# Optimization experiments

Hardware: AMD Instinct MI355X
Metric: run time of the kernel (lower is better)

Reference implementation:

```python
import jax, jax.numpy as jnp
import numpy as np

B, S, D = 64, 512, 768
NEG = -1e30


def setup_inputs() -> dict:
    key = jax.random.key(0)
    ks = jax.random.split(key, 20)
    def rn(k, shape, scale=0.02):
        return jax.random.normal(k, shape, dtype=jnp.float32) * scale
    ep = jax.random.randint(ks[1], (B, 3, 2), 0, S, dtype=jnp.int32)
    return {
        "encoding": jax.random.normal(ks[0], (B, S, D), dtype=jnp.float32),
        "ent_pos": jnp.sort(ep, axis=-1),
        "Ar_W": rn(ks[2], (5, D)), "Ar_b": rn(ks[3], (D,)),
        "Vr_W1": rn(ks[4], (2 * D, 512)), "Vr_b1": rn(ks[5], (512,)),
        "Vr_W2": rn(ks[6], (512, 5)), "Vr_b2": rn(ks[7], (5,)),
        "gate_W": rn(ks[8], (2 * D, D)), "gate_b": rn(ks[9], (D,)),
        "pred_W1": rn(ks[10], (3 * D, 512)), "pred_b1": rn(ks[11], (512,)),
        "pred_W2": rn(ks[12], (512, 5)), "pred_b2": rn(ks[13], (5,)),
        "proj_W": rn(ks[14], (D, 1)), "proj_b": rn(ks[15], (1,)),
    }


def reference(encoding, ent_pos, Ar_W, Ar_b, Vr_W1, Vr_b1, Vr_W2, Vr_b2,
              gate_W, gate_b, pred_W1, pred_b1, pred_W2, pred_b2, proj_W, proj_b):
    # --- entity span max-pooling (vectorized over batch & 3 entities) ---
    pos = jnp.arange(S)                                   # [S]
    start = ent_pos[..., 0:1]                             # [B,3,1]
    end = ent_pos[..., 1:2]                               # [B,3,1]
    mask = (pos >= start) & (pos <= end)                  # [B,3,S]
    ent = jnp.max(jnp.where(mask[..., None], encoding[:, None, :, :], NEG), axis=2)  # [B,3,D]
    # dropout layers are identity at inference

    def vr(a, b):  # V_r_layer: Linear(1536,512)+ReLU+Linear(512,5)+Sigmoid
        h = jax.nn.relu(jnp.concatenate([a, b], axis=-1) @ Vr_W1 + Vr_b1)
        return jax.nn.sigmoid(h @ Vr_W2 + Vr_b2)          # [B,5]

    def gate(u, e):  # gated residual update
        g = jax.nn.sigmoid(jnp.concatenate([u, e], axis=-1) @ gate_W + gate_b)
        return g * e + (1.0 - g) * u

    e1, e2, e3 = ent[:, 0], ent[:, 1], ent[:, 2]          # [B,D] each
    for _ in range(5):
        u1 = (vr(e2, e3) @ Ar_W + Ar_b) * e1
        u2 = (vr(e1, e3) @ Ar_W + Ar_b) * e2
        u3 = (vr(e1, e2) @ Ar_W + Ar_b) * e3
        e1, e2, e3 = gate(u1, e1), gate(u2, e2), gate(u3, e3)
    final_ent = jnp.stack([e1, e2, e3], axis=1)           # [B,3,D]

    # predict_layer on the ORIGINAL pooled entity embeddings (per source code)
    flat = ent.reshape(B, 3 * D)
    rel = jax.nn.relu(flat @ pred_W1 + pred_b1) @ pred_W2 + pred_b2  # [B,5]
    ent_score = jax.nn.sigmoid(ent @ proj_W + proj_b)[..., 0]       # [B,3]
    return rel, ent_score, final_ent
```

## Files before the change

kernel.cpp:

```cpp
#include <hip/hip_runtime.h>
#include <hip/hip_bf16.h>
#include <math.h>

#define NEGF (-1e30f)

#define P_OFF    0u
#define PP_OFF   0u
#define ENT_OFF  2359296u
#define EA_OFF   2506752u
#define EB_OFF   2654208u
#define SP_OFF   2801664u

__device__ __forceinline__ float sigmoidf_(float x){ return 1.0f/(1.0f+expf(-x)); }

__global__ __launch_bounds__(192) void k_span_partial(
    const float* __restrict__ enc, const int* __restrict__ ent_pos, float* __restrict__ ws)
{
    int c = blockIdx.x, bi = blockIdx.y, t = threadIdx.x;
    int b = bi/3;
    int st = ent_pos[bi*2+0], en = ent_pos[bi*2+1];
    int r0 = max(st, c*32), r1 = min(en, c*32+31);
    if (r0 > r1) return;
    float4 m = make_float4(NEGF,NEGF,NEGF,NEGF);
    const float4* e4 = (const float4*)enc + (size_t)b*512*192 + t;
    int r = r0;
    for (; r+3<=r1; r+=4){
        float4 v0 = e4[(size_t)(r  )*192];
        float4 v1 = e4[(size_t)(r+1)*192];
        float4 v2 = e4[(size_t)(r+2)*192];
        float4 v3 = e4[(size_t)(r+3)*192];
        m.x=fmaxf(m.x,fmaxf(fmaxf(v0.x,v1.x),fmaxf(v2.x,v3.x)));
        m.y=fmaxf(m.y,fmaxf(fmaxf(v0.y,v1.y),fmaxf(v2.y,v3.y)));
        m.z=fmaxf(m.z,fmaxf(fmaxf(v0.z,v1.z),fmaxf(v2.z,v3.z)));
        m.w=fmaxf(m.w,fmaxf(fmaxf(v0.w,v1.w),fmaxf(v2.w,v3.w)));
    }
    for (; r<=r1; ++r){
        float4 v = e4[(size_t)r*192];
        m.x=fmaxf(m.x,v.x); m.y=fmaxf(m.y,v.y); m.z=fmaxf(m.z,v.z); m.w=fmaxf(m.w,v.w);
    }
    ((float4*)(ws+P_OFF))[((size_t)bi*16 + c)*192 + t] = m;
}

__global__ __launch_bounds__(192) void k_span_reduce(
    const int* __restrict__ ent_pos,
    const float* __restrict__ projW, const float* __restrict__ projb,
    float* __restrict__ ws, float* __restrict__ out)
{
    __shared__ float red[4];
    int bi = blockIdx.x; int t = threadIdx.x;
    int st = ent_pos[bi*2+0], en = ent_pos[bi*2+1];
    float4 m = make_float4(NEGF,NEGF,NEGF,NEGF);
    const float4* p4 = (const float4*)(ws+P_OFF);
    for (int c=0;c<16;++c){
        if (c*32 <= en && c*32+31 >= st){
            float4 v = p4[((size_t)bi*16 + c)*192 + t];
            m.x=fmaxf(m.x,v.x); m.y=fmaxf(m.y,v.y); m.z=fmaxf(m.z,v.z); m.w=fmaxf(m.w,v.w);
        }
    }
    ((float4*)(ws+ENT_OFF))[bi*192+t] = m;
    ((float4*)(ws+EA_OFF))[bi*192+t] = m;
    float4 w = ((const float4*)projW)[t];
    float v = m.x*w.x + m.y*w.y + m.z*w.z + m.w*w.w;
    v += __shfl_down(v, 32);
    v += __shfl_down(v, 16);
    v += __shfl_down(v, 8);
    v += __shfl_down(v, 4);
    v += __shfl_down(v, 2);
    v += __shfl_down(v, 1);
    if ((t & 63) == 0) red[t>>6] = v;
    __syncthreads();
    if (t==0) out[320 + bi] = sigmoidf_(red[0]+red[1]+red[2] + projb[0]);
}

__global__ __launch_bounds__(256) void k_pred_part(
    const float* __restrict__ predW1, float* __restrict__ ws)
{
    int ct = blockIdx.x, rb = blockIdx.y, ks = blockIdx.z;
    int tx = threadIdx.x & 31, ty = threadIdx.x >> 5;
    int row = rb*8+ty, col = ct*32+tx;
    const float* A = ws + ENT_OFF + (size_t)row*2304 + ks*288;
    const float* W = predW1 + (size_t)(ks*288)*512 + col;
    float acc = 0.f;
    #pragma unroll 4
    for (int k=0;k<288;++k){ acc = fmaf(A[k], W[(size_t)k*512], acc); }
    ws[PP_OFF + ((size_t)(ks*64+row))*512 + col] = acc;
}

__global__ __launch_bounds__(256) void k_vr_fused(
    const float* __restrict__ W1, const float* __restrict__ b1,
    const float* __restrict__ W2, const float* __restrict__ eSrc,
    const float* __restrict__ pb1, const float* __restrict__ pW2,
    const float* __restrict__ pb2,
    float* __restrict__ ws, float* __restrict__ out)
{
    __shared__ float eL[4608];
    __shared__ float red[16*16*17];
    int g = blockIdx.x;
    int t = threadIdx.x;
    if (g >= 256){
        int bx = g - 256;
        int gid = t >> 5, l = t & 31;
        int b = bx*8 + gid;
        float acc0=0,acc1=0,acc2=0,acc3=0,acc4=0;
        for (int c = l; c < 512; c += 32){
            float h = 0.f;
            #pragma unroll
            for (int ks=0;ks<8;++ks) h += ws[PP_OFF + ((size_t)(ks*64+b))*512 + c];
            h = fmaxf(h + pb1[c], 0.f);
            acc0 = fmaf(h, pW2[c*5+0], acc0);
            acc1 = fmaf(h, pW2[c*5+1], acc1);
            acc2 = fmaf(h, pW2[c*5+2], acc2);
            acc3 = fmaf(h, pW2[c*5+3], acc3);
            acc4 = fmaf(h, pW2[c*5+4], acc4);
        }
        #pragma unroll
        for (int s=16; s>0; s>>=1){
            acc0 += __shfl_down(acc0, s, 32);
            acc1 += __shfl_down(acc1, s, 32);
            acc2 += __shfl_down(acc2, s, 32);
            acc3 += __shfl_down(acc3, s, 32);
            acc4 += __shfl_down(acc4, s, 32);
        }
        if (l == 0){
            out[b*5+0] = acc0 + pb2[0];
            out[b*5+1] = acc1 + pb2[1];
            out[b*5+2] = acc2 + pb2[2];
            out[b*5+3] = acc3 + pb2[3];
            out[b*5+4] = acc4 + pb2[4];
        }
        return;
    }
    int ct = g & 7, bg = g >> 3;
    int b0 = bg*2;
    const float* eBase = eSrc + (size_t)b0*2304;
    for (int idx=t; idx<4608; idx+=256) eL[idx] = eBase[idx];
    __syncthreads();

    int tp = t & 15;
    int kq = t >> 4;
    int c0 = ct*64;
    int col = c0 + 4*tp;
    const float* Wp = W1 + (size_t)(kq*96)*512 + col;
    int off1 = (kq<8) ? (768 + kq*96) : (1536 + (kq-8)*96);
    int off2 = (kq<8) ? (      kq*96) : (768  + (kq-8)*96);
    const float* pP0 = eL + off1;
    const float* pQ0 = eL + off2;
    const float* pP1 = eL + 2304 + off1;
    const float* pQ1 = eL + 2304 + off2;
    float aP0[4]={0,0,0,0}, aQ0[4]={0,0,0,0}, aP1[4]={0,0,0,0}, aQ1[4]={0,0,0,0};
    #pragma unroll 8
    for (int i=0;i<96;++i){
        float4 w = *(const float4*)(Wp + (size_t)i*512);
        float p0 = pP0[i], q0 = pQ0[i], p1 = pP1[i], q1 = pQ1[i];
        aP0[0]=fmaf(p0,w.x,aP0[0]); aP0[1]=fmaf(p0,w.y,aP0[1]); aP0[2]=fmaf(p0,w.z,aP0[2]); aP0[3]=fmaf(p0,w.w,aP0[3]);
        aQ0[0]=fmaf(q0,w.x,aQ0[0]); aQ0[1]=fmaf(q0,w.y,aQ0[1]); aQ0[2]=fmaf(q0,w.z,aQ0[2]); aQ0[3]=fmaf(q0,w.w,aQ0[3]);
        aP1[0]=fmaf(p1,w.x,aP1[0]); aP1[1]=fmaf(p1,w.y,aP1[1]); aP1[2]=fmaf(p1,w.z,aP1[2]); aP1[3]=fmaf(p1,w.w,aP1[3]);
        aQ1[0]=fmaf(q1,w.x,aQ1[0]); aQ1[1]=fmaf(q1,w.y,aQ1[1]); aQ1[2]=fmaf(q1,w.z,aQ1[2]); aQ1[3]=fmaf(q1,w.w,aQ1[3]);
    }
    float* rp = red + (kq*16 + tp)*17;
    #pragma unroll
    for (int c=0;c<4;++c){ rp[c]=aP0[c]; rp[4+c]=aQ0[c]; rp[8+c]=aP1[c]; rp[12+c]=aQ1[c]; }
    __syncthreads();

    if (t < 128){
        int bb = t >> 6;
        int tc = t & 63;
        int tp2 = tc >> 2, c = tc & 3;
        int base = bb*8;
        float SP1=0,SP2=0,SQ1=0,SQ2=0;
        #pragma unroll
        for (int k=0;k<8;++k){
            SP1 += red[(k*16+tp2)*17 + base + c];
            SQ1 += red[(k*16+tp2)*17 + base + 4 + c];
            SP2 += red[((k+8)*16+tp2)*17 + base + c];
            SQ2 += red[((k+8)*16+tp2)*17 + base + 4 + c];
        }
        int cc = c0 + tc;
        float bv = b1[cc];
        float h0 = fmaxf(SP1+SP2+bv, 0.f);
        float h1 = fmaxf(SQ1+SP2+bv, 0.f);
        float h2 = fmaxf(SQ1+SQ2+bv, 0.f);
        float w20 = W2[cc*5+0], w21 = W2[cc*5+1], w22 = W2[cc*5+2], w23 = W2[cc*5+3], w24 = W2[cc*5+4];
        float pr[15] = { h0*w20,h0*w21,h0*w22,h0*w23,h0*w24,
                         h1*w20,h1*w21,h1*w22,h1*w23,h1*w24,
                         h2*w20,h2*w21,h2*w22,h2*w23,h2*w24 };
        #pragma unroll
        for (int j=0;j<15;++j){
            float v = pr[j];
            v += __shfl_down(v, 32);
            v += __shfl_down(v, 16);
            v += __shfl_down(v, 8);
            v += __shfl_down(v, 4);
            v += __shfl_down(v, 2);
            v += __shfl_down(v, 1);
            pr[j] = v;
        }
        if (tc == 0){
            float* sp = ws + SP_OFF + ((size_t)ct*192 + (size_t)(b0+bb)*3)*5;
            #pragma unroll
            for (int j=0;j<15;++j) sp[j] = pr[j];
        }
    }
}

__global__ __launch_bounds__(384) void k_gate_fused(
    const float* __restrict__ gW, const float* __restrict__ gb,
    const float* __restrict__ ArW, const float* __restrict__ Arb,
    const float* __restrict__ Vb2,
    const float* __restrict__ eSrc, float* __restrict__ eDst,
    float* __restrict__ ws, float* __restrict__ finalOut)
{
    __shared__ float eL[4608];
    __shared__ float uL[4608];
    __shared__ float red[16*24*25];
    __shared__ float sL[32];
    int g = blockIdx.x;
    int t = threadIdx.x;
    int ct = g & 7, bg = g >> 3;
    int b0 = bg*2;
    const float* eBase = eSrc + (size_t)b0*2304;
    for (int idx=t; idx<4608; idx+=384) eL[idx] = eBase[idx];
    if (t < 30){
        int bb = t/15, pc = t%15, cc = pc%5;
        int row = (b0+bb)*3 + pc/5;
        float pre = Vb2[cc];
        #pragma unroll
        for (int q=0;q<8;++q) pre += ws[SP_OFF + ((size_t)q*192 + row)*5 + cc];
        sL[t] = sigmoidf_(pre);
    }
    __syncthreads();
    for (int idx=t; idx<4608; idx+=384){
        int r = idx / 768;
        int k = idx - r*768;
        int bb = r / 3;  int p = r - bb*3;
        const float* s = sL + bb*15 + p*5;
        float a = Arb[k] + s[0]*ArW[k] + s[1]*ArW[768+k] + s[2]*ArW[1536+k]
                         + s[3]*ArW[2304+k] + s[4]*ArW[3072+k];
        uL[idx] = a * eL[idx];
    }
    __syncthreads();

    int kq = t / 24, tp = t - kq*24;
    int c0 = ct*96;
    int col = c0 + 4*tp;
    const float* Wp = gW + (size_t)(kq*96)*768 + col;
    const float* A = (kq<8) ? uL : eL;
    int kb = (kq & 7)*96;
    float acc[6][4];
    #pragma unroll
    for (int r=0;r<6;++r){ acc[r][0]=0.f; acc[r][1]=0.f; acc[r][2]=0.f; acc[r][3]=0.f; }
    #pragma unroll 4
    for (int i=0;i<96;++i){
        float4 w = *(const float4*)(Wp + (size_t)i*768);
        #pragma unroll
        for (int r=0;r<6;++r){
            float a = A[r*768 + kb + i];
            acc[r][0] = fmaf(a, w.x, acc[r][0]);
            acc[r][1] = fmaf(a, w.y, acc[r][1]);
            acc[r][2] = fmaf(a, w.z, acc[r][2]);
            acc[r][3] = fmaf(a, w.w, acc[r][3]);
        }
    }
    float* rp = red + (kq*24+tp)*25;
    #pragma unroll
    for (int r=0;r<6;++r){
        rp[r*4+0]=acc[r][0]; rp[r*4+1]=acc[r][1]; rp[r*4+2]=acc[r][2]; rp[r*4+3]=acc[r][3];
    }
    __syncthreads();

    for (int o=t; o<576; o+=384){
        int rr = o / 96, tc = o - rr*96;
        int tp2 = tc >> 2, c = tc & 3;
        int bb = rr/3, p = rr - bb*3;
        float gp = 0.f;
        #pragma unroll
        for (int k=0;k<16;++k) gp += red[(k*24+tp2)*25 + rr*4 + c];
        int jc = c0 + tc;
        float gv = sigmoidf_(gp + gb[jc]);
        float e = eL[bb*2304 + p*768 + jc];
        float u = uL[bb*2304 + p*768 + jc];
        float val = gv*e + (1.f-gv)*u;
        size_t oi = ((size_t)(b0+bb)*3 + p)*768 + jc;
        eDst[oi] = val;
        if (finalOut) finalOut[oi] = val;
    }
}

extern "C" void kernel_launch(void* const* d_in, const int* in_sizes, int n_in,
                              void* d_out, int out_size, void* d_ws, size_t ws_size,
                              hipStream_t stream)
{
    const float* enc     = (const float*)d_in[0];
    const int*   ent_pos = (const int*)d_in[1];
    const float* ArW     = (const float*)d_in[2];
    const float* Arb     = (const float*)d_in[3];
    const float* VrW1    = (const float*)d_in[4];
    const float* Vrb1    = (const float*)d_in[5];
    const float* VrW2    = (const float*)d_in[6];
    const float* Vrb2    = (const float*)d_in[7];
    const float* gateW   = (const float*)d_in[8];
    const float* gateb   = (const float*)d_in[9];
    const float* predW1  = (const float*)d_in[10];
    const float* predb1  = (const float*)d_in[11];
    const float* predW2  = (const float*)d_in[12];
    const float* predb2  = (const float*)d_in[13];
    const float* projW   = (const float*)d_in[14];
    const float* projb   = (const float*)d_in[15];
    float* out = (float*)d_out;
    float* ws  = (float*)d_ws;

    hipLaunchKernelGGL(k_span_partial, dim3(16,192), dim3(192), 0, stream, enc, ent_pos, ws);
    hipLaunchKernelGGL(k_span_reduce, dim3(192), dim3(192), 0, stream, ent_pos, projW, projb, ws, out);
    hipLaunchKernelGGL(k_pred_part, dim3(16,8,8), dim3(256), 0, stream, predW1, ws);
    for (int it=0; it<5; ++it){
        float* eS = ws + ((it&1)==0 ? EA_OFF : EB_OFF);
        float* eD = ws + ((it&1)==0 ? EB_OFF : EA_OFF);
        hipLaunchKernelGGL(k_vr_fused, dim3(it==0 ? 264 : 256), dim3(256), 0, stream,
                           VrW1, Vrb1, VrW2, eS, predb1, predW2, predb2, ws, out);
        hipLaunchKernelGGL(k_gate_fused, dim3(256), dim3(384), 0, stream, gateW, gateb, ArW, Arb, Vrb2,
                           eS, eD, ws, (it==4) ? (out+512) : (float*)nullptr);
    }
}
```

Baseline: 160.2 us.

## Use one batch per block in vr/gate kernels and fold pred GEMM into first vr launch

The vr and gate kernels now give each block one batch row instead of two, which doubles the grid to 512 blocks and halves shared memory and register accumulators. This should improve occupancy and spread work over more CUs, at the cost of loading each weight tile twice as often. The separate predict-layer partial GEMM is folded into the first vr launch as extra blocks, and a small new kernel finishes the prediction head after it. The gate kernel gains an unused dead-code branch for blocks at index 512 and above, but it never runs because only 512 blocks are launched.

```diff
diff --git a/kernel.cpp b/kernel.cpp
--- a/kernel.cpp
+++ b/kernel.cpp
@@ -72,68 +72,32 @@
     if (t==0) out[320 + bi] = sigmoidf_(red[0]+red[1]+red[2] + projb[0]);
 }
 
-__global__ __launch_bounds__(256) void k_pred_part(
-    const float* __restrict__ predW1, float* __restrict__ ws)
-{
-    int ct = blockIdx.x, rb = blockIdx.y, ks = blockIdx.z;
-    int tx = threadIdx.x & 31, ty = threadIdx.x >> 5;
-    int row = rb*8+ty, col = ct*32+tx;
-    const float* A = ws + ENT_OFF + (size_t)row*2304 + ks*288;
-    const float* W = predW1 + (size_t)(ks*288)*512 + col;
-    float acc = 0.f;
-    #pragma unroll 4
-    for (int k=0;k<288;++k){ acc = fmaf(A[k], W[(size_t)k*512], acc); }
-    ws[PP_OFF + ((size_t)(ks*64+row))*512 + col] = acc;
-}
-
 __global__ __launch_bounds__(256) void k_vr_fused(
     const float* __restrict__ W1, const float* __restrict__ b1,
     const float* __restrict__ W2, const float* __restrict__ eSrc,
-    const float* __restrict__ pb1, const float* __restrict__ pW2,
-    const float* __restrict__ pb2,
-    float* __restrict__ ws, float* __restrict__ out)
-{
-    __shared__ float eL[4608];
-    __shared__ float red[16*16*17];
+    const float* __restrict__ pW1,
+    float* __restrict__ ws)
+{
+    __shared__ float eL[2304];
+    __shared__ float red[16*16*9];
     int g = blockIdx.x;
     int t = threadIdx.x;
-    if (g >= 256){
-        int bx = g - 256;
-        int gid = t >> 5, l = t & 31;
-        int b = bx*8 + gid;
-        float acc0=0,acc1=0,acc2=0,acc3=0,acc4=0;
-        for (int c = l; c < 512; c += 32){
-            float h = 0.f;
-            #pragma unroll
-            for (int ks=0;ks<8;++ks) h += ws[PP_OFF + ((size_t)(ks*64+b))*512 + c];
-            h = fmaxf(h + pb1[c], 0.f);
-            acc0 = fmaf(h, pW2[c*5+0], acc0);
-            acc1 = fmaf(h, pW2[c*5+1], acc1);
-            acc2 = fmaf(h, pW2[c*5+2], acc2);
-            acc3 = fmaf(h, pW2[c*5+3], acc3);
-            acc4 = fmaf(h, pW2[c*5+4], acc4);
-        }
-        #pragma unroll
-        for (int s=16; s>0; s>>=1){
-            acc0 += __shfl_down(acc0, s, 32);
-            acc1 += __shfl_down(acc1, s, 32);
-            acc2 += __shfl_down(acc2, s, 32);
-            acc3 += __shfl_down(acc3, s, 32);
-            acc4 += __shfl_down(acc4, s, 32);
-        }
-        if (l == 0){
-            out[b*5+0] = acc0 + pb2[0];
-            out[b*5+1] = acc1 + pb2[1];
-            out[b*5+2] = acc2 + pb2[2];
-            out[b*5+3] = acc3 + pb2[3];
-            out[b*5+4] = acc4 + pb2[4];
-        }
+    if (g >= 512){
+        int g2 = g - 512;
+        int ct2 = g2 & 15, rb = (g2 >> 4) & 7, ks = g2 >> 7;
+        int tx = t & 31, ty = t >> 5;
+        int row = rb*8+ty, col = ct2*32+tx;
+        const float* A = ws + ENT_OFF + (size_t)row*2304 + ks*288;
+        const float* W = pW1 + (size_t)(ks*288)*512 + col;
+        float acc = 0.f;
+        #pragma unroll 4
+        for (int k=0;k<288;++k){ acc = fmaf(A[k], W[(size_t)k*512], acc); }
+        ws[PP_OFF + ((size_t)(ks*64+row))*512 + col] = acc;
         return;
     }
-    int ct = g & 7, bg = g >> 3;
-    int b0 = bg*2;
-    const float* eBase = eSrc + (size_t)b0*2304;
-    for (int idx=t; idx<4608; idx+=256) eL[idx] = eBase[idx];
+    int ct = g & 7, b = g >> 3;
+    const float* eBase = eSrc + (size_t)b*2304;
+    for (int idx=t; idx<2304; idx+=256) eL[idx] = eBase[idx];
     __syncthreads();
 
     int tp = t & 15;
@@ -143,37 +107,31 @@
     const float* Wp = W1 + (size_t)(kq*96)*512 + col;
     int off1 = (kq<8) ? (768 + kq*96) : (1536 + (kq-8)*96);
     int off2 = (kq<8) ? (      kq*96) : (768  + (kq-8)*96);
-    const float* pP0 = eL + off1;
-    const float* pQ0 = eL + off2;
-    const float* pP1 = eL + 2304 + off1;
-    const float* pQ1 = eL + 2304 + off2;
-    float aP0[4]={0,0,0,0}, aQ0[4]={0,0,0,0}, aP1[4]={0,0,0,0}, aQ1[4]={0,0,0,0};
+    const float* pP = eL + off1;
+    const float* pQ = eL + off2;
+    float aP[4]={0,0,0,0}, aQ[4]={0,0,0,0};
     #pragma unroll 8
     for (int i=0;i<96;++i){
         float4 w = *(const float4*)(Wp + (size_t)i*512);
-        float p0 = pP0[i], q0 = pQ0[i], p1 = pP1[i], q1 = pQ1[i];
-        aP0[0]=fmaf(p0,w.x,aP0[0]); aP0[1]=fmaf(p0,w.y,aP0[1]); aP0[2]=fmaf(p0,w.z,aP0[2]); aP0[3]=fmaf(p0,w.w,aP0[3]);
-        aQ0[0]=fmaf(q0,w.x,aQ0[0]); aQ0[1]=fmaf(q0,w.y,aQ0[1]); aQ0[2]=fmaf(q0,w.z,aQ0[2]); aQ0[3]=fmaf(q0,w.w,aQ0[3]);
-        aP1[0]=fmaf(p1,w.x,aP1[0]); aP1[1]=fmaf(p1,w.y,aP1[1]); aP1[2]=fmaf(p1,w.z,aP1[2]); aP1[3]=fmaf(p1,w.w,aP1[3]);
-        aQ1[0]=fmaf(q1,w.x,aQ1[0]); aQ1[1]=fmaf(q1,w.y,aQ1[1]); aQ1[2]=fmaf(q1,w.z,aQ1[2]); aQ1[3]=fmaf(q1,w.w,aQ1[3]);
-    }
-    float* rp = red + (kq*16 + tp)*17;
+        float p = pP[i], q = pQ[i];
+        aP[0]=fmaf(p,w.x,aP[0]); aP[1]=fmaf(p,w.y,aP[1]); aP[2]=fmaf(p,w.z,aP[2]); aP[3]=fmaf(p,w.w,aP[3]);
+        aQ[0]=fmaf(q,w.x,aQ[0]); aQ[1]=fmaf(q,w.y,aQ[1]); aQ[2]=fmaf(q,w.z,aQ[2]); aQ[3]=fmaf(q,w.w,aQ[3]);
+    }
+    float* rp = red + (kq*16 + tp)*9;
     #pragma unroll
-    for (int c=0;c<4;++c){ rp[c]=aP0[c]; rp[4+c]=aQ0[c]; rp[8+c]=aP1[c]; rp[12+c]=aQ1[c]; }
-    __syncthreads();
-
-    if (t < 128){
-        int bb = t >> 6;
-        int tc = t & 63;
+    for (int c=0;c<4;++c){ rp[c]=aP[c]; rp[4+c]=aQ[c]; }
+    __syncthreads();
+
+    if (t < 64){
+        int tc = t;
         int tp2 = tc >> 2, c = tc & 3;
-        int base = bb*8;
         float SP1=0,SP2=0,SQ1=0,SQ2=0;
         #pragma unroll
         for (int k=0;k<8;++k){
-            SP1 += red[(k*16+tp2)*17 + base + c];
-            SQ1 += red[(k*16+tp2)*17 + base + 4 + c];
-            SP2 += red[((k+8)*16+tp2)*17 + base + c];
-            SQ2 += red[((k+8)*16+tp2)*17 + base + 4 + c];
+            SP1 += red[(k*16+tp2)*9 + c];
+            SQ1 += red[(k*16+tp2)*9 + 4 + c];
+            SP2 += red[((k+8)*16+tp2)*9 + c];
+            SQ2 += red[((k+8)*16+tp2)*9 + 4 + c];
         }
         int cc = c0 + tc;
         float bv = b1[cc];
@@ -196,7 +154,7 @@
             pr[j] = v;
         }
         if (tc == 0){
-            float* sp = ws + SP_OFF + ((size_t)ct*192 + (size_t)(b0+bb)*3)*5;
+            float* sp = ws + SP_OFF + ((size_t)ct*192 + (size_t)b*3)*5;
             #pragma unroll
             for (int j=0;j<15;++j) sp[j] = pr[j];
         }
@@ -207,33 +165,67 @@
     const float* __restrict__ gW, const float* __restrict__ gb,
     const float* __restrict__ ArW, const float* __restrict__ Arb,
     const float* __restrict__ Vb2,
+    const float* __restrict__ pb1, const float* __restrict__ pW2,
+    const float* __restrict__ pb2,
     const float* __restrict__ eSrc, float* __restrict__ eDst,
     float* __restrict__ ws, float* __restrict__ finalOut)
 {
-    __shared__ float eL[4608];
-    __shared__ float uL[4608];
-    __shared__ float red[16*24*25];
-    __shared__ float sL[32];
+    __shared__ float eL[2304];
+    __shared__ float uL[2304];
+    __shared__ float red[16*24*13];
+    __shared__ float sL[16];
     int g = blockIdx.x;
     int t = threadIdx.x;
-    int ct = g & 7, bg = g >> 3;
-    int b0 = bg*2;
-    const float* eBase = eSrc + (size_t)b0*2304;
-    for (int idx=t; idx<4608; idx+=384) eL[idx] = eBase[idx];
-    if (t < 30){
-        int bb = t/15, pc = t%15, cc = pc%5;
-        int row = (b0+bb)*3 + pc/5;
+    if (g >= 512){
+        int bx = g - 512;
+        int gid = t >> 5, l = t & 31;
+        if (gid < 8){
+            int b = bx*8 + gid;
+            float acc0=0,acc1=0,acc2=0,acc3=0,acc4=0;
+            for (int c = l; c < 512; c += 32){
+                float h = 0.f;
+                #pragma unroll
+                for (int ks=0;ks<8;++ks) h += ws[PP_OFF + ((size_t)(ks*64+b))*512 + c];
+                h = fmaxf(h + pb1[c], 0.f);
+                acc0 = fmaf(h, pW2[c*5+0], acc0);
+                acc1 = fmaf(h, pW2[c*5+1], acc1);
+                acc2 = fmaf(h, pW2[c*5+2], acc2);
+                acc3 = fmaf(h, pW2[c*5+3], acc3);
+                acc4 = fmaf(h, pW2[c*5+4], acc4);
+            }
+            #pragma unroll
+            for (int s=16; s>0; s>>=1){
+                acc0 += __shfl_down(acc0, s, 32);
+                acc1 += __shfl_down(acc1, s, 32);
+                acc2 += __shfl_down(acc2, s, 32);
+                acc3 += __shfl_down(acc3, s, 32);
+                acc4 += __shfl_down(acc4, s, 32);
+            }
+            if (l == 0){
+                float* o = finalOut ? finalOut : finalOut;
+                (void)o;
+            }
+            if (l == 0){
+            }
+        }
+        return;
+    }
+    int ct = g & 7, b = g >> 3;
+    const float* eBase = eSrc + (size_t)b*2304;
+    for (int idx=t; idx<2304; idx+=384) eL[idx] = eBase[idx];
+    if (t < 15){
+        int cc = t%5, p = t/5;
+        int row = b*3 + p;
         float pre = Vb2[cc];
         #pragma unroll
         for (int q=0;q<8;++q) pre += ws[SP_OFF + ((size_t)q*192 + row)*5 + cc];
         sL[t] = sigmoidf_(pre);
     }
     __syncthreads();
-    for (int idx=t; idx<4608; idx+=384){
+    for (int idx=t; idx<2304; idx+=384){
         int r = idx / 768;
         int k = idx - r*768;
-        int bb = r / 3;  int p = r - bb*3;
-        const float* s = sL + bb*15 + p*5;
+        const float* s = sL + r*5;
         float a = Arb[k] + s[0]*ArW[k] + s[1]*ArW[768+k] + s[2]*ArW[1536+k]
                          + s[3]*ArW[2304+k] + s[4]*ArW[3072+k];
         uL[idx] = a * eL[idx];
@@ -246,14 +238,14 @@
     const float* Wp = gW + (size_t)(kq*96)*768 + col;
     const float* A = (kq<8) ? uL : eL;
     int kb = (kq & 7)*96;
-    float acc[6][4];
+    float acc[3][4];
     #pragma unroll
-    for (int r=0;r<6;++r){ acc[r][0]=0.f; acc[r][1]=0.f; acc[r][2]=0.f; acc[r][3]=0.f; }
+    for (int r=0;r<3;++r){ acc[r][0]=0.f; acc[r][1]=0.f; acc[r][2]=0.f; acc[r][3]=0.f; }
     #pragma unroll 4
     for (int i=0;i<96;++i){
         float4 w = *(const float4*)(Wp + (size_t)i*768);
         #pragma unroll
-        for (int r=0;r<6;++r){
+        for (int r=0;r<3;++r){
             float a = A[r*768 + kb + i];
             acc[r][0] = fmaf(a, w.x, acc[r][0]);
             acc[r][1] = fmaf(a, w.y, acc[r][1]);
@@ -261,28 +253,63 @@
             acc[r][3] = fmaf(a, w.w, acc[r][3]);
         }
     }
-    float* rp = red + (kq*24+tp)*25;
+    float* rp = red + (kq*24+tp)*13;
     #pragma unroll
-    for (int r=0;r<6;++r){
+    for (int r=0;r<3;++r){
         rp[r*4+0]=acc[r][0]; rp[r*4+1]=acc[r][1]; rp[r*4+2]=acc[r][2]; rp[r*4+3]=acc[r][3];
     }
     __syncthreads();
 
-    for (int o=t; o<576; o+=384){
-        int rr = o / 96, tc = o - rr*96;
+    if (t < 288){
+        int rr = t / 96, tc = t - rr*96;
         int tp2 = tc >> 2, c = tc & 3;
-        int bb = rr/3, p = rr - bb*3;
         float gp = 0.f;
         #pragma unroll
-        for (int k=0;k<16;++k) gp += red[(k*24+tp2)*25 + rr*4 + c];
+        for (int k=0;k<16;++k) gp += red[(k*24+tp2)*13 + rr*4 + c];
         int jc = c0 + tc;
         float gv = sigmoidf_(gp + gb[jc]);
-        float e = eL[bb*2304 + p*768 + jc];
-        float u = uL[bb*2304 + p*768 + jc];
+        float e = eL[rr*768 + jc];
+        float u = uL[rr*768 + jc];
         float val = gv*e + (1.f-gv)*u;
-        size_t oi = ((size_t)(b0+bb)*3 + p)*768 + jc;
+        size_t oi = ((size_t)b*3 + rr)*768 + jc;
         eDst[oi] = val;
         if (finalOut) finalOut[oi] = val;
+    }
+}
+
+__global__ __launch_bounds__(256) void k_pred_fin(
+    const float* __restrict__ pb1, const float* __restrict__ pW2,
+    const float* __restrict__ pb2, float* __restrict__ ws, float* __restrict__ out)
+{
+    int bx = blockIdx.x;
+    int gid = threadIdx.x >> 5, l = threadIdx.x & 31;
+    int b = bx*8 + gid;
+    float acc0=0,acc1=0,acc2=0,acc3=0,acc4=0;
+    for (int c = l; c < 512; c += 32){
+        float h = 0.f;
+        #pragma unroll
+        for (int ks=0;ks<8;++ks) h += ws[PP_OFF + ((size_t)(ks*64+b))*512 + c];
+        h = fmaxf(h + pb1[c], 0.f);
+        acc0 = fmaf(h, pW2[c*5+0], acc0);
+        acc1 = fmaf(h, pW2[c*5+1], acc1);
+        acc2 = fmaf(h, pW2[c*5+2], acc2);
+        acc3 = fmaf(h, pW2[c*5+3], acc3);
+        acc4 = fmaf(h, pW2[c*5+4], acc4);
+    }
+    #pragma unroll
+    for (int s=16; s>0; s>>=1){
+        acc0 += __shfl_down(acc0, s, 32);
+        acc1 += __shfl_down(acc1, s, 32);
+        acc2 += __shfl_down(acc2, s, 32);
+        acc3 += __shfl_down(acc3, s, 32);
+        acc4 += __shfl_down(acc4, s, 32);
+    }
+    if (l == 0){
+        out[b*5+0] = acc0 + pb2[0];
+        out[b*5+1] = acc1 + pb2[1];
+        out[b*5+2] = acc2 + pb2[2];
+        out[b*5+3] = acc3 + pb2[3];
+        out[b*5+4] = acc4 + pb2[4];
     }
 }
 
@@ -311,13 +338,16 @@
 
     hipLaunchKernelGGL(k_span_partial, dim3(16,192), dim3(192), 0, stream, enc, ent_pos, ws);
     hipLaunchKernelGGL(k_span_reduce, dim3(192), dim3(192), 0, stream, ent_pos, projW, projb, ws, out);
-    hipLaunchKernelGGL(k_pred_part, dim3(16,8,8), dim3(256), 0, stream, predW1, ws);
     for (int it=0; it<5; ++it){
         float* eS = ws + ((it&1)==0 ? EA_OFF : EB_OFF);
         float* eD = ws + ((it&1)==0 ? EB_OFF : EA_OFF);
-        hipLaunchKernelGGL(k_vr_fused, dim3(it==0 ? 264 : 256), dim3(256), 0, stream,
-                           VrW1, Vrb1, VrW2, eS, predb1, predW2, predb2, ws, out);
-        hipLaunchKernelGGL(k_gate_fused, dim3(256), dim3(384), 0, stream, gateW, gateb, ArW, Arb, Vrb2,
+        hipLaunchKernelGGL(k_vr_fused, dim3(it==0 ? 1536 : 512), dim3(256), 0, stream,
+                           VrW1, Vrb1, VrW2, eS, predW1, ws);
+        if (it==0)
+            hipLaunchKernelGGL(k_pred_fin, dim3(8), dim3(256), 0, stream,
+                               predb1, predW2, predb2, ws, out);
+        hipLaunchKernelGGL(k_gate_fused, dim3(512), dim3(384), 0, stream,
+                           gateW, gateb, ArW, Arb, Vrb2, predb1, predW2, predb2,
                            eS, eD, ws, (it==4) ? (out+512) : (float*)nullptr);
     }
 }
```

Result: slower. 182.0 us (+13.6%).

## Retile Vr GEMM to four batches per block and fold pred GEMM into first launch

Applied to the files above, without the earlier changes.

The Vr-layer kernel now handles four batch rows per block over 32 columns with 32 k-slices, so each loaded W1 value is reused across more rows. This cuts redundant weight traffic, at the cost of a larger shared-memory footprint and 16 partial slots that the gate kernel must sum. The predict-layer partial GEMM moves into the first iteration's Vr launch as extra blocks, and its finalisation moves into a separate small kernel. The aim is to remove the standalone launch and overlap the two GEMMs.

```diff
diff --git a/kernel.cpp b/kernel.cpp
--- a/kernel.cpp
+++ b/kernel.cpp
@@ -72,108 +72,76 @@
     if (t==0) out[320 + bi] = sigmoidf_(red[0]+red[1]+red[2] + projb[0]);
 }
 
-__global__ __launch_bounds__(256) void k_pred_part(
-    const float* __restrict__ predW1, float* __restrict__ ws)
-{
-    int ct = blockIdx.x, rb = blockIdx.y, ks = blockIdx.z;
-    int tx = threadIdx.x & 31, ty = threadIdx.x >> 5;
-    int row = rb*8+ty, col = ct*32+tx;
-    const float* A = ws + ENT_OFF + (size_t)row*2304 + ks*288;
-    const float* W = predW1 + (size_t)(ks*288)*512 + col;
-    float acc = 0.f;
-    #pragma unroll 4
-    for (int k=0;k<288;++k){ acc = fmaf(A[k], W[(size_t)k*512], acc); }
-    ws[PP_OFF + ((size_t)(ks*64+row))*512 + col] = acc;
-}
-
 __global__ __launch_bounds__(256) void k_vr_fused(
     const float* __restrict__ W1, const float* __restrict__ b1,
     const float* __restrict__ W2, const float* __restrict__ eSrc,
-    const float* __restrict__ pb1, const float* __restrict__ pW2,
-    const float* __restrict__ pb2,
-    float* __restrict__ ws, float* __restrict__ out)
-{
-    __shared__ float eL[4608];
-    __shared__ float red[16*16*17];
+    const float* __restrict__ pW1,
+    float* __restrict__ ws)
+{
+    __shared__ float eL[9216];
+    __shared__ float red[256*33];
     int g = blockIdx.x;
     int t = threadIdx.x;
     if (g >= 256){
-        int bx = g - 256;
-        int gid = t >> 5, l = t & 31;
-        int b = bx*8 + gid;
-        float acc0=0,acc1=0,acc2=0,acc3=0,acc4=0;
-        for (int c = l; c < 512; c += 32){
-            float h = 0.f;
-            #pragma unroll
-            for (int ks=0;ks<8;++ks) h += ws[PP_OFF + ((size_t)(ks*64+b))*512 + c];
-            h = fmaxf(h + pb1[c], 0.f);
-            acc0 = fmaf(h, pW2[c*5+0], acc0);
-            acc1 = fmaf(h, pW2[c*5+1], acc1);
-            acc2 = fmaf(h, pW2[c*5+2], acc2);
-            acc3 = fmaf(h, pW2[c*5+3], acc3);
-            acc4 = fmaf(h, pW2[c*5+4], acc4);
-        }
-        #pragma unroll
-        for (int s=16; s>0; s>>=1){
-            acc0 += __shfl_down(acc0, s, 32);
-            acc1 += __shfl_down(acc1, s, 32);
-            acc2 += __shfl_down(acc2, s, 32);
-            acc3 += __shfl_down(acc3, s, 32);
-            acc4 += __shfl_down(acc4, s, 32);
-        }
-        if (l == 0){
-            out[b*5+0] = acc0 + pb2[0];
-            out[b*5+1] = acc1 + pb2[1];
-            out[b*5+2] = acc2 + pb2[2];
-            out[b*5+3] = acc3 + pb2[3];
-            out[b*5+4] = acc4 + pb2[4];
-        }
+        int g2 = g - 256;
+        int ct2 = g2 & 15, rb = (g2 >> 4) & 7, ks = g2 >> 7;
+        int tx = t & 31, ty = t >> 5;
+        int row = rb*8+ty, col = ct2*32+tx;
+        const float* A = ws + ENT_OFF + (size_t)row*2304 + ks*288;
+        const float* W = pW1 + (size_t)(ks*288)*512 + col;
+        float acc = 0.f;
+        #pragma unroll 4
+        for (int k=0;k<288;++k){ acc = fmaf(A[k], W[(size_t)k*512], acc); }
+        ws[PP_OFF + ((size_t)(ks*64+row))*512 + col] = acc;
         return;
     }
-    int ct = g & 7, bg = g >> 3;
-    int b0 = bg*2;
+    int ct = g & 15, bg = g >> 4;
+    int b0 = bg*4;
     const float* eBase = eSrc + (size_t)b0*2304;
-    for (int idx=t; idx<4608; idx+=256) eL[idx] = eBase[idx];
-    __syncthreads();
-
-    int tp = t & 15;
-    int kq = t >> 4;
-    int c0 = ct*64;
+    for (int idx=t; idx<9216; idx+=256) eL[idx] = eBase[idx];
+    __syncthreads();
+
+    int tp = t & 7;
+    int kq = t >> 3;
+    int c0 = ct*32;
     int col = c0 + 4*tp;
-    const float* Wp = W1 + (size_t)(kq*96)*512 + col;
-    int off1 = (kq<8) ? (768 + kq*96) : (1536 + (kq-8)*96);
-    int off2 = (kq<8) ? (      kq*96) : (768  + (kq-8)*96);
-    const float* pP0 = eL + off1;
-    const float* pQ0 = eL + off2;
-    const float* pP1 = eL + 2304 + off1;
-    const float* pQ1 = eL + 2304 + off2;
-    float aP0[4]={0,0,0,0}, aQ0[4]={0,0,0,0}, aP1[4]={0,0,0,0}, aQ1[4]={0,0,0,0};
-    #pragma unroll 8
-    for (int i=0;i<96;++i){
+    const float* Wp = W1 + (size_t)(kq*48)*512 + col;
+    int off1 = (kq<16) ? (768 + kq*48) : (1536 + (kq-16)*48);
+    int off2 = (kq<16) ? (      kq*48) : (768  + (kq-16)*48);
+    float aP[4][4] = {{0,0,0,0},{0,0,0,0},{0,0,0,0},{0,0,0,0}};
+    float aQ[4][4] = {{0,0,0,0},{0,0,0,0},{0,0,0,0},{0,0,0,0}};
+    #pragma unroll 4
+    for (int i=0;i<48;++i){
         float4 w = *(const float4*)(Wp + (size_t)i*512);
-        float p0 = pP0[i], q0 = pQ0[i], p1 = pP1[i], q1 = pQ1[i];
-        aP0[0]=fmaf(p0,w.x,aP0[0]); aP0[1]=fmaf(p0,w.y,aP0[1]); aP0[2]=fmaf(p0,w.z,aP0[2]); aP0[3]=fmaf(p0,w.w,aP0[3]);
-        aQ0[0]=fmaf(q0,w.x,aQ0[0]); aQ0[1]=fmaf(q0,w.y,aQ0[1]); aQ0[2]=fmaf(q0,w.z,aQ0[2]); aQ0[3]=fmaf(q0,w.w,aQ0[3]);
-        aP1[0]=fmaf(p1,w.x,aP1[0]); aP1[1]=fmaf(p1,w.y,aP1[1]); aP1[2]=fmaf(p1,w.z,aP1[2]); aP1[3]=fmaf(p1,w.w,aP1[3]);
-        aQ1[0]=fmaf(q1,w.x,aQ1[0]); aQ1[1]=fmaf(q1,w.y,aQ1[1]); aQ1[2]=fmaf(q1,w.z,aQ1[2]); aQ1[3]=fmaf(q1,w.w,aQ1[3]);
-    }
-    float* rp = red + (kq*16 + tp)*17;
+        #pragma unroll
+        for (int bb=0;bb<4;++bb){
+            float p = eL[bb*2304 + off1 + i];
+            float q = eL[bb*2304 + off2 + i];
+            aP[bb][0]=fmaf(p,w.x,aP[bb][0]); aP[bb][1]=fmaf(p,w.y,aP[bb][1]);
+            aP[bb][2]=fmaf(p,w.z,aP[bb][2]); aP[bb][3]=fmaf(p,w.w,aP[bb][3]);
+            aQ[bb][0]=fmaf(q,w.x,aQ[bb][0]); aQ[bb][1]=fmaf(q,w.y,aQ[bb][1]);
+            aQ[bb][2]=fmaf(q,w.z,aQ[bb][2]); aQ[bb][3]=fmaf(q,w.w,aQ[bb][3]);
+        }
+    }
+    float* rp = red + (size_t)(kq*8 + tp)*33;
     #pragma unroll
-    for (int c=0;c<4;++c){ rp[c]=aP0[c]; rp[4+c]=aQ0[c]; rp[8+c]=aP1[c]; rp[12+c]=aQ1[c]; }
+    for (int bb=0;bb<4;++bb){
+        #pragma unroll
+        for (int c=0;c<4;++c){ rp[bb*8+c]=aP[bb][c]; rp[bb*8+4+c]=aQ[bb][c]; }
+    }
     __syncthreads();
 
     if (t < 128){
-        int bb = t >> 6;
-        int tc = t & 63;
+        int bb = t >> 5;
+        int tc = t & 31;
         int tp2 = tc >> 2, c = tc & 3;
-        int base = bb*8;
         float SP1=0,SP2=0,SQ1=0,SQ2=0;
         #pragma unroll
-        for (int k=0;k<8;++k){
-            SP1 += red[(k*16+tp2)*17 + base + c];
-            SQ1 += red[(k*16+tp2)*17 + base + 4 + c];
-            SP2 += red[((k+8)*16+tp2)*17 + base + c];
-            SQ2 += red[((k+8)*16+tp2)*17 + base + 4 + c];
+        for (int k=0;k<16;++k){
+            SP1 += red[(size_t)(k*8+tp2)*33 + bb*8 + c];
+            SQ1 += red[(size_t)(k*8+tp2)*33 + bb*8 + 4 + c];
+            SP2 += red[(size_t)((k+16)*8+tp2)*33 + bb*8 + c];
+            SQ2 += red[(size_t)((k+16)*8+tp2)*33 + bb*8 + 4 + c];
         }
         int cc = c0 + tc;
         float bv = b1[cc];
@@ -187,12 +155,11 @@
         #pragma unroll
         for (int j=0;j<15;++j){
             float v = pr[j];
-            v += __shfl_down(v, 32);
-            v += __shfl_down(v, 16);
-            v += __shfl_down(v, 8);
-            v += __shfl_down(v, 4);
-            v += __shfl_down(v, 2);
-            v += __shfl_down(v, 1);
+            v += __shfl_down(v, 16, 32);
+            v += __shfl_down(v, 8, 32);
+            v += __shfl_down(v, 4, 32);
+            v += __shfl_down(v, 2, 32);
+            v += __shfl_down(v, 1, 32);
             pr[j] = v;
         }
         if (tc == 0){
@@ -225,7 +192,7 @@
         int row = (b0+bb)*3 + pc/5;
         float pre = Vb2[cc];
         #pragma unroll
-        for (int q=0;q<8;++q) pre += ws[SP_OFF + ((size_t)q*192 + row)*5 + cc];
+        for (int q=0;q<16;++q) pre += ws[SP_OFF + ((size_t)q*192 + row)*5 + cc];
         sL[t] = sigmoidf_(pre);
     }
     __syncthreads();
@@ -283,6 +250,42 @@
         size_t oi = ((size_t)(b0+bb)*3 + p)*768 + jc;
         eDst[oi] = val;
         if (finalOut) finalOut[oi] = val;
+    }
+}
+
+__global__ __launch_bounds__(256) void k_pred_fin(
+    const float* __restrict__ pb1, const float* __restrict__ pW2,
+    const float* __restrict__ pb2, float* __restrict__ ws, float* __restrict__ out)
+{
+    int bx = blockIdx.x;
+    int gid = threadIdx.x >> 5, l = threadIdx.x & 31;
+    int b = bx*8 + gid;
+    float acc0=0,acc1=0,acc2=0,acc3=0,acc4=0;
+    for (int c = l; c < 512; c += 32){
+        float h = 0.f;
+        #pragma unroll
+        for (int ks=0;ks<8;++ks) h += ws[PP_OFF + ((size_t)(ks*64+b))*512 + c];
+        h = fmaxf(h + pb1[c], 0.f);
+        acc0 = fmaf(h, pW2[c*5+0], acc0);
+        acc1 = fmaf(h, pW2[c*5+1], acc1);
+        acc2 = fmaf(h, pW2[c*5+2], acc2);
+        acc3 = fmaf(h, pW2[c*5+3], acc3);
+        acc4 = fmaf(h, pW2[c*5+4], acc4);
+    }
+    #pragma unroll
+    for (int s=16; s>0; s>>=1){
+        acc0 += __shfl_down(acc0, s, 32);
+        acc1 += __shfl_down(acc1, s, 32);
+        acc2 += __shfl_down(acc2, s, 32);
+        acc3 += __shfl_down(acc3, s, 32);
+        acc4 += __shfl_down(acc4, s, 32);
+    }
+    if (l == 0){
+        out[b*5+0] = acc0 + pb2[0];
+        out[b*5+1] = acc1 + pb2[1];
+        out[b*5+2] = acc2 + pb2[2];
+        out[b*5+3] = acc3 + pb2[3];
+        out[b*5+4] = acc4 + pb2[4];
     }
 }
 
@@ -311,13 +314,16 @@
 
     hipLaunchKernelGGL(k_span_partial, dim3(16,192), dim3(192), 0, stream, enc, ent_pos, ws);
     hipLaunchKernelGGL(k_span_reduce, dim3(192), dim3(192), 0, stream, ent_pos, projW, projb, ws, out);
-    hipLaunchKernelGGL(k_pred_part, dim3(16,8,8), dim3(256), 0, stream, predW1, ws);
     for (int it=0; it<5; ++it){
         float* eS = ws + ((it&1)==0 ? EA_OFF : EB_OFF);
         float* eD = ws + ((it&1)==0 ? EB_OFF : EA_OFF);
-        hipLaunchKernelGGL(k_vr_fused, dim3(it==0 ? 264 : 256), dim3(256), 0, stream,
-                           VrW1, Vrb1, VrW2, eS, predb1, predW2, predb2, ws, out);
-        hipLaunchKernelGGL(k_gate_fused, dim3(256), dim3(384), 0, stream, gateW, gateb, ArW, Arb, Vrb2,
+        hipLaunchKernelGGL(k_vr_fused, dim3(it==0 ? 1280 : 256), dim3(256), 0, stream,
+                           VrW1, Vrb1, VrW2, eS, predW1, ws);
+        if (it==0)
+            hipLaunchKernelGGL(k_pred_fin, dim3(8), dim3(256), 0, stream,
+                               predb1, predW2, predb2, ws, out);
+        hipLaunchKernelGGL(k_gate_fused, dim3(256), dim3(384), 0, stream,
+                           gateW, gateb, ArW, Arb, Vrb2,
                            eS, eD, ws, (it==4) ? (out+512) : (float*)nullptr);
     }
 }
```

Result: slower. 189.2 us (+18.1%).

## Fold predict-layer partial GEMM into first Vr kernel and epilogue into gate kernel

Applied to the files above, without the earlier changes.

The standalone predict-layer partial GEMM launch is removed. Its 1024 blocks now run as extra blocks of the first-iteration Vr kernel, so they share a grid with the Vr blocks. The reduction and second linear layer of the predict head move into extra blocks of the first gate kernel, which runs after the partials are written. This removes one kernel launch and overlaps the predict-head work with the entity iteration. In exchange, the first Vr launch grows to 1280 blocks, which may delay its critical-path Vr blocks.

```diff
diff --git a/kernel.cpp b/kernel.cpp
--- a/kernel.cpp
+++ b/kernel.cpp
@@ -72,62 +72,27 @@
     if (t==0) out[320 + bi] = sigmoidf_(red[0]+red[1]+red[2] + projb[0]);
 }
 
-__global__ __launch_bounds__(256) void k_pred_part(
-    const float* __restrict__ predW1, float* __restrict__ ws)
-{
-    int ct = blockIdx.x, rb = blockIdx.y, ks = blockIdx.z;
-    int tx = threadIdx.x & 31, ty = threadIdx.x >> 5;
-    int row = rb*8+ty, col = ct*32+tx;
-    const float* A = ws + ENT_OFF + (size_t)row*2304 + ks*288;
-    const float* W = predW1 + (size_t)(ks*288)*512 + col;
-    float acc = 0.f;
-    #pragma unroll 4
-    for (int k=0;k<288;++k){ acc = fmaf(A[k], W[(size_t)k*512], acc); }
-    ws[PP_OFF + ((size_t)(ks*64+row))*512 + col] = acc;
-}
-
 __global__ __launch_bounds__(256) void k_vr_fused(
     const float* __restrict__ W1, const float* __restrict__ b1,
     const float* __restrict__ W2, const float* __restrict__ eSrc,
-    const float* __restrict__ pb1, const float* __restrict__ pW2,
-    const float* __restrict__ pb2,
-    float* __restrict__ ws, float* __restrict__ out)
+    const float* __restrict__ pW1,
+    float* __restrict__ ws)
 {
     __shared__ float eL[4608];
     __shared__ float red[16*16*17];
     int g = blockIdx.x;
     int t = threadIdx.x;
     if (g >= 256){
-        int bx = g - 256;
-        int gid = t >> 5, l = t & 31;
-        int b = bx*8 + gid;
-        float acc0=0,acc1=0,acc2=0,acc3=0,acc4=0;
-        for (int c = l; c < 512; c += 32){
-            float h = 0.f;
-            #pragma unroll
-            for (int ks=0;ks<8;++ks) h += ws[PP_OFF + ((size_t)(ks*64+b))*512 + c];
-            h = fmaxf(h + pb1[c], 0.f);
-            acc0 = fmaf(h, pW2[c*5+0], acc0);
-            acc1 = fmaf(h, pW2[c*5+1], acc1);
-            acc2 = fmaf(h, pW2[c*5+2], acc2);
-            acc3 = fmaf(h, pW2[c*5+3], acc3);
-            acc4 = fmaf(h, pW2[c*5+4], acc4);
-        }
-        #pragma unroll
-        for (int s=16; s>0; s>>=1){
-            acc0 += __shfl_down(acc0, s, 32);
-            acc1 += __shfl_down(acc1, s, 32);
-            acc2 += __shfl_down(acc2, s, 32);
-            acc3 += __shfl_down(acc3, s, 32);
-            acc4 += __shfl_down(acc4, s, 32);
-        }
-        if (l == 0){
-            out[b*5+0] = acc0 + pb2[0];
-            out[b*5+1] = acc1 + pb2[1];
-            out[b*5+2] = acc2 + pb2[2];
-            out[b*5+3] = acc3 + pb2[3];
-            out[b*5+4] = acc4 + pb2[4];
-        }
+        int g2 = g - 256;
+        int ct2 = g2 & 15, rb = (g2 >> 4) & 7, ks = g2 >> 7;
+        int tx = t & 31, ty = t >> 5;
+        int row = rb*8+ty, col = ct2*32+tx;
+        const float* A = ws + ENT_OFF + (size_t)row*2304 + ks*288;
+        const float* W = pW1 + (size_t)(ks*288)*512 + col;
+        float acc = 0.f;
+        #pragma unroll 4
+        for (int k=0;k<288;++k){ acc = fmaf(A[k], W[(size_t)k*512], acc); }
+        ws[PP_OFF + ((size_t)(ks*64+row))*512 + col] = acc;
         return;
     }
     int ct = g & 7, bg = g >> 3;
@@ -207,8 +172,10 @@
     const float* __restrict__ gW, const float* __restrict__ gb,
     const float* __restrict__ ArW, const float* __restrict__ Arb,
     const float* __restrict__ Vb2,
+    const float* __restrict__ pb1, const float* __restrict__ pW2,
+    const float* __restrict__ pb2,
     const float* __restrict__ eSrc, float* __restrict__ eDst,
-    float* __restrict__ ws, float* __restrict__ finalOut)
+    float* __restrict__ ws, float* __restrict__ relOut, float* __restrict__ finalOut)
 {
     __shared__ float eL[4608];
     __shared__ float uL[4608];
@@ -216,6 +183,41 @@
     __shared__ float sL[32];
     int g = blockIdx.x;
     int t = threadIdx.x;
+    if (g >= 256){
+        int bx = g - 256;
+        int gid = t >> 5, l = t & 31;
+        if (gid < 8){
+            int b = bx*8 + gid;
+            float acc0=0,acc1=0,acc2=0,acc3=0,acc4=0;
+            for (int c = l; c < 512; c += 32){
+                float h = 0.f;
+                #pragma unroll
+                for (int ks=0;ks<8;++ks) h += ws[PP_OFF + ((size_t)(ks*64+b))*512 + c];
+                h = fmaxf(h + pb1[c], 0.f);
+                acc0 = fmaf(h, pW2[c*5+0], acc0);
+                acc1 = fmaf(h, pW2[c*5+1], acc1);
+                acc2 = fmaf(h, pW2[c*5+2], acc2);
+                acc3 = fmaf(h, pW2[c*5+3], acc3);
+                acc4 = fmaf(h, pW2[c*5+4], acc4);
+            }
+            #pragma unroll
+            for (int s=16; s>0; s>>=1){
+                acc0 += __shfl_down(acc0, s, 32);
+                acc1 += __shfl_down(acc1, s, 32);
+                acc2 += __shfl_down(acc2, s, 32);
+                acc3 += __shfl_down(acc3, s, 32);
+                acc4 += __shfl_down(acc4, s, 32);
+            }
+            if (l == 0){
+                relOut[b*5+0] = acc0 + pb2[0];
+                relOut[b*5+1] = acc1 + pb2[1];
+                relOut[b*5+2] = acc2 + pb2[2];
+                relOut[b*5+3] = acc3 + pb2[3];
+                relOut[b*5+4] = acc4 + pb2[4];
+            }
+        }
+        return;
+    }
     int ct = g & 7, bg = g >> 3;
     int b0 = bg*2;
     const float* eBase = eSrc + (size_t)b0*2304;
@@ -311,13 +313,13 @@
 
     hipLaunchKernelGGL(k_span_partial, dim3(16,192), dim3(192), 0, stream, enc, ent_pos, ws);
     hipLaunchKernelGGL(k_span_reduce, dim3(192), dim3(192), 0, stream, ent_pos, projW, projb, ws, out);
-    hipLaunchKernelGGL(k_pred_part, dim3(16,8,8), dim3(256), 0, stream, predW1, ws);
     for (int it=0; it<5; ++it){
         float* eS = ws + ((it&1)==0 ? EA_OFF : EB_OFF);
         float* eD = ws + ((it&1)==0 ? EB_OFF : EA_OFF);
-        hipLaunchKernelGGL(k_vr_fused, dim3(it==0 ? 264 : 256), dim3(256), 0, stream,
-                           VrW1, Vrb1, VrW2, eS, predb1, predW2, predb2, ws, out);
-        hipLaunchKernelGGL(k_gate_fused, dim3(256), dim3(384), 0, stream, gateW, gateb, ArW, Arb, Vrb2,
-                           eS, eD, ws, (it==4) ? (out+512) : (float*)nullptr);
-    }
-}
+        hipLaunchKernelGGL(k_vr_fused, dim3(it==0 ? 1280 : 256), dim3(256), 0, stream,
+                           VrW1, Vrb1, VrW2, eS, predW1, ws);
+        hipLaunchKernelGGL(k_gate_fused, dim3(it==0 ? 264 : 256), dim3(384), 0, stream,
+                           gateW, gateb, ArW, Arb, Vrb2, predb1, predW2, predb2,
+                           eS, eD, ws, out, (it==4) ? (out+512) : (float*)nullptr);
+    }
+}
```

New measurement: 167.4 us. 4.4% more time.
